# Kernel tuning notes

Measured on AMD Instinct MI355X. Metric: run time of the kernel, lower is better.

The kernel has to match this reference:

```python
import jax, jax.numpy as jnp
import numpy as np

B, A, N = 4, 256, 64
NCB, NF, NSB, DIMS = 128, 128, 50, 3
CUTOFF = 5.0
LOG2 = 0.6931471805599453


def ssp(x):
    # shifted softplus: softplus(x) - ln(2)
    return jax.nn.softplus(x) - LOG2


def mlp2(x, W1, b1, W2, b2):
    # Dense(act=ssp) -> Dense(linear)
    return ssp(x @ W1 + b1) @ W2 + b2


def setup_inputs():
    key = jax.random.key(0)
    ks = jax.random.split(key, 32)

    def w(k, shape):
        return jax.random.normal(k, shape, jnp.float32) / np.sqrt(shape[0]).astype(np.float32)

    return {
        "xi": jax.random.normal(ks[0], (B, A, NCB), jnp.float32),
        "r_ij": jax.random.uniform(ks[1], (B, A, N), jnp.float32) * CUTOFF,
        "cos_ij": jax.random.normal(ks[2], (B, A, N, DIMS), jnp.float32),
        "f_ij": jax.random.normal(ks[3], (B, A, N, NSB), jnp.float32),
        "neighbor_mask": jnp.ones((B, A, N), jnp.float32),
        "filt_W1": w(ks[4], (NSB, NF)), "filt_b1": jnp.zeros((NF,), jnp.float32),
        "filt_W2": w(ks[5], (NF, NF)), "filt_b2": jnp.zeros((NF,), jnp.float32),
        "in2f_W": w(ks[6], (NCB, NF)),
        "f2out_W": w(ks[7], (NF, NF)), "f2out_b": jnp.zeros((NF,), jnp.float32),
        "atom_W1": w(ks[8], (NF, NF)), "atom_b1": jnp.zeros((NF,), jnp.float32),
        "atom_W2": w(ks[9], (NF, NCB)), "atom_b2": jnp.zeros((NCB,), jnp.float32),
        "pair_W1": w(ks[10], (NF, NF)), "pair_b1": jnp.zeros((NF,), jnp.float32),
        "pair_W2": w(ks[11], (NF, NCB)), "pair_b2": jnp.zeros((NCB,), jnp.float32),
        "env_W1": w(ks[12], (NF, NF)), "env_b1": jnp.zeros((NF,), jnp.float32),
        "env_W2": w(ks[13], (NF, NCB)), "env_b2": jnp.zeros((NCB,), jnp.float32),
        "neighbors": jax.random.randint(ks[14], (B, A, N), 0, A),
    }


def reference(xi, r_ij, cos_ij, f_ij, neighbor_mask,
              filt_W1, filt_b1, filt_W2, filt_b2, in2f_W, f2out_W, f2out_b,
              atom_W1, atom_b1, atom_W2, atom_b2,
              pair_W1, pair_b1, pair_W2, pair_b2,
              env_W1, env_b1, env_W2, env_b2, neighbors):
    bidx = jnp.arange(B)[:, None, None]
    # --- FTLayer: filter net on Gaussian-expanded distances, cosine cutoff ---
    Wf = ssp(f_ij @ filt_W1 + filt_b1) @ filt_W2 + filt_b2            # [B,A,N,NF]
    C = 0.5 * (jnp.cos(r_ij * (jnp.pi / CUTOFF)) + 1.0) * (r_ij < CUTOFF)
    Wf = Wf * C[..., None]
    yj = (xi @ in2f_W)[bidx, neighbors]                               # gather -> [B,A,N,NF]
    v = ssp((yj * Wf) @ f2out_W + f2out_b)                            # [B,A,N,NF]
    # --- atom-wise channel (masked neighbor sum) ---
    vi = jnp.sum(v * neighbor_mask[..., None], axis=2)                # [B,A,NF]
    vi = mlp2(vi, atom_W1, atom_b1, atom_W2, atom_b2)                 # [B,A,NCB]
    # --- pair tensor: outer product with cosine basis ---
    vij = mlp2(v, pair_W1, pair_b1, pair_W2, pair_b2)                 # [B,A,N,NCB]
    Vij = vij[..., None] * cos_ij[..., None, :]                       # [B,A,N,NCB,3]
    # --- environment tensor: masked agg then second-order neighbor gather ---
    vik = mlp2(v, env_W1, env_b1, env_W2, env_b2)                     # [B,A,N,NCB]
    Vik = jnp.sum(vik[..., None] * cos_ij[..., None, :]
                  * neighbor_mask[..., None, None], axis=2)           # [B,A,NCB,3]
    Vjl = Vik[bidx, neighbors]                                        # [B,A,N,NCB,3]
    V = Vij + Vik[:, :, None] + Vjl                                   # [B,A,N,NCB,3]
    return vi, V
```

## Files before the change

kernel.cpp:

```cpp
#include <hip/hip_runtime.h>
#include <hip/hip_bf16.h>
#include <math.h>

#define B 4
#define A 256
#define NN 64
#define NCB 128
#define NF 128
#define NSB 50
#define BA (B*A)
#define PAIRS (BA*NN)

typedef __bf16 bf;
typedef __attribute__((ext_vector_type(8))) __bf16 bfrag8;
typedef __attribute__((ext_vector_type(4))) float ffrag4;

__device__ __attribute__((aligned(16))) bf    g_yib[BA*NF];
__device__ __attribute__((aligned(16))) bf    g_vij[(size_t)PAIRS*NCB];
__device__ __attribute__((aligned(16))) float g_vik[BA*NCB*3];
__device__ __attribute__((aligned(16))) bf g_tf1[NF*64];
__device__ __attribute__((aligned(16))) bf g_tf2[NF*NF];
__device__ __attribute__((aligned(16))) bf g_tfo[NF*NF];
__device__ __attribute__((aligned(16))) bf g_tp1[NF*NF];
__device__ __attribute__((aligned(16))) bf g_tp2[NF*NF];
__device__ __attribute__((aligned(16))) bf g_te1[NF*NF];
__device__ __attribute__((aligned(16))) bf g_te2[NF*NF];

__device__ __forceinline__ float ssp(float x){
    float e = __expf(-fabsf(x));
    return fmaxf(x, 0.f) + __logf(1.f + e) - 0.6931471805599453f;
}

__global__ __launch_bounds__(256)
void k_wt(const float* __restrict__ f1, const float* __restrict__ f2,
          const float* __restrict__ fo, const float* __restrict__ p1,
          const float* __restrict__ p2, const float* __restrict__ e1,
          const float* __restrict__ e2){
    int s = blockIdx.x >> 3, part = blockIdx.x & 7;
    const float* src; bf* dst; int kb, realK;
    if (s == 0){ src = f1; dst = g_tf1; kb = 6; realK = NSB; }
    else {
        kb = 7; realK = 128;
        src = (s==1)?f2:(s==2)?fo:(s==3)?p1:(s==4)?p2:(s==5)?e1:e2;
        dst = (s==1)?g_tf2:(s==2)?g_tfo:(s==3)?g_tp1:(s==4)?g_tp2:(s==5)?g_te1:g_te2;
    }
    int total = NF << kb;
    int chunk = total >> 3;
    int end = (part + 1) * chunk;
    for (int e = part*chunk + threadIdx.x; e < end; e += 256){
        int n = e >> kb, k = e & ((1<<kb)-1);
        dst[e] = (k < realK) ? (bf)src[k*NF + n] : (bf)0.f;
    }
}

__global__ __launch_bounds__(NF)
void k_yi(const float* __restrict__ xi, const float* __restrict__ W){
    int row = blockIdx.x, f = threadIdx.x;
    __shared__ float x[NCB];
    x[f] = xi[row*NCB + f];
    __syncthreads();
    float s = 0.f;
    #pragma unroll 16
    for (int c = 0; c < NCB; c++) s += x[c]*W[c*NF + f];
    g_yib[row*NF + f] = (bf)s;
}

__device__ __forceinline__ void stage_w128(bf* __restrict__ sW, const bf* __restrict__ g,
                                           int half, int tid){
    #pragma unroll
    for (int i = 0; i < 4; i++){
        int r  = i*16 + (tid >> 4);
        int cp = (tid & 15)*8;
        *(bfrag8*)&sW[r*136 + cp] = *(const bfrag8*)&g[(half*64 + r)*128 + cp];
    }
}
__device__ __forceinline__ void stage_w64(bf* __restrict__ sW, const bf* __restrict__ g,
                                          int half, int tid){
    #pragma unroll
    for (int i = 0; i < 2; i++){
        int r  = i*32 + (tid >> 3);
        int cp = (tid & 7)*8;
        *(bfrag8*)&sW[r*72 + cp] = *(const bfrag8*)&g[(half*64 + r)*64 + cp];
    }
}
__device__ __forceinline__ void gemm4(const bf* __restrict__ sW, const bfrag8 afr[4],
                                      ffrag4 acc[4], int q, int c16){
    #pragma unroll
    for (int nt = 0; nt < 4; nt++){
        ffrag4 a = {0.f,0.f,0.f,0.f};
        #pragma unroll
        for (int kt = 0; kt < 4; kt++){
            bfrag8 bv = *(const bfrag8*)&sW[(nt*16 + c16)*136 + kt*32 + q*8];
            a = __builtin_amdgcn_mfma_f32_16x16x32_bf16(afr[kt], bv, a, 0, 0, 0);
        }
        acc[nt] = a;
    }
}
__device__ __forceinline__ void gemm2(const bf* __restrict__ sW, const bfrag8 afr[2],
                                      ffrag4 acc[4], int q, int c16){
    #pragma unroll
    for (int nt = 0; nt < 4; nt++){
        ffrag4 a = {0.f,0.f,0.f,0.f};
        #pragma unroll
        for (int kt = 0; kt < 2; kt++){
            bfrag8 bv = *(const bfrag8*)&sW[(nt*16 + c16)*72 + kt*32 + q*8];
            a = __builtin_amdgcn_mfma_f32_16x16x32_bf16(afr[kt], bv, a, 0, 0, 0);
        }
        acc[nt] = a;
    }
}

__global__ __launch_bounds__(256, 3)
void k_main(const float* __restrict__ r_ij, const float* __restrict__ cos_ij,
            const float* __restrict__ f_ij, const float* __restrict__ mask,
            const int* __restrict__ neighbors,
            const float* __restrict__ fb1, const float* __restrict__ fb2,
            const float* __restrict__ f2b,
            const float* __restrict__ aW1, const float* __restrict__ ab1,
            const float* __restrict__ aW2, const float* __restrict__ ab2,
            const float* __restrict__ pb1, const float* __restrict__ pb2,
            const float* __restrict__ eb1, const float* __restrict__ eb2,
            float* __restrict__ out_vi){
    const int tid  = threadIdx.x;
    const int ba   = blockIdx.x;
    const int b    = ba >> 8;
    const int w    = tid >> 6;
    const int lane = tid & 63;
    const int q    = lane >> 4;
    const int c16  = lane & 15;
    const int arow = w*16 + c16;

    __shared__ __attribute__((aligned(16))) char sWb[64*136*2];
    bf* const sW = (bf*)sWb;
    __shared__ __attribute__((aligned(16))) bf sA [64*136];
    __shared__ __attribute__((aligned(16))) bf sA2[64*136];
    __shared__ float sCosM[64*4];
    __shared__ float sCr[64];
    __shared__ int   sJb[64];

    #pragma unroll
    for (int i = 0; i < 16; i++){
        int e = tid + i*256;
        int row = e >> 6, col = e & 63;
        float v = (col < NSB) ? f_ij[(ba*64 + row)*NSB + col] : 0.f;
        sA2[row*136 + col] = (bf)v;
    }
    if (tid < 64){
        int p = ba*64 + tid;
        sCosM[tid*4+0] = cos_ij[p*3+0];
        sCosM[tid*4+1] = cos_ij[p*3+1];
        sCosM[tid*4+2] = cos_ij[p*3+2];
        sCosM[tid*4+3] = mask[p];
        float r = r_ij[p];
        sCr[tid] = (r < 5.f) ? 0.5f*(__cosf(r*0.62831853071795864769f) + 1.f) : 0.f;
        int j = neighbors[p] & (A-1);
        sJb[tid] = (b*A + j)*NF;
    }
    __syncthreads();

    bfrag8 afr4[4]; bfrag8 afr2[2]; ffrag4 acc[4];

    #pragma unroll
    for (int kt = 0; kt < 2; kt++) afr2[kt] = *(const bfrag8*)&sA2[arow*136 + kt*32 + q*8];
    #pragma unroll
    for (int half = 0; half < 2; half++){
        if (half) __syncthreads();
        stage_w64(sW, g_tf1, half, tid);
        __syncthreads();
        gemm2(sW, afr2, acc, q, c16);
        #pragma unroll
        for (int nt = 0; nt < 4; nt++){
            int col = (half*4 + nt)*16 + c16;
            float bias = fb1[col];
            #pragma unroll
            for (int rg = 0; rg < 4; rg++){
                int row = w*16 + q*4 + rg;
                sA[row*136 + col] = (bf)ssp(acc[nt][rg] + bias);
            }
        }
    }
    __syncthreads();

    #pragma unroll
    for (int kt = 0; kt < 4; kt++) afr4[kt] = *(const bfrag8*)&sA[arow*136 + kt*32 + q*8];
    #pragma unroll
    for (int half = 0; half < 2; half++){
        if (half) __syncthreads();
        stage_w128(sW, g_tf2, half, tid);
        __syncthreads();
        gemm4(sW, afr4, acc, q, c16);
        #pragma unroll
        for (int nt = 0; nt < 4; nt++){
            int col = (half*4 + nt)*16 + c16;
            float bias = fb2[col];
            #pragma unroll
            for (int rg = 0; rg < 4; rg++){
                int row = w*16 + q*4 + rg;
                float wf = (acc[nt][rg] + bias) * sCr[row];
                float u  = (float)g_yib[sJb[row] + col] * wf;
                sA[row*136 + col] = (bf)u;
            }
        }
    }
    __syncthreads();

    float vsAll[8];
    #pragma unroll
    for (int t = 0; t < 8; t++) vsAll[t] = 0.f;
    #pragma unroll
    for (int kt = 0; kt < 4; kt++) afr4[kt] = *(const bfrag8*)&sA[arow*136 + kt*32 + q*8];
    #pragma unroll
    for (int half = 0; half < 2; half++){
        if (half) __syncthreads();
        stage_w128(sW, g_tfo, half, tid);
        __syncthreads();
        gemm4(sW, afr4, acc, q, c16);
        #pragma unroll
        for (int nt = 0; nt < 4; nt++){
            int col = (half*4 + nt)*16 + c16;
            float bias = f2b[col];
            #pragma unroll
            for (int rg = 0; rg < 4; rg++){
                int row = w*16 + q*4 + rg;
                float v = ssp(acc[nt][rg] + bias);
                sA[row*136 + col] = (bf)v;
                vsAll[half*4 + nt] += v * sCosM[row*4+3];
            }
        }
    }
    __syncthreads();

    #pragma unroll
    for (int kt = 0; kt < 4; kt++) afr4[kt] = *(const bfrag8*)&sA[arow*136 + kt*32 + q*8];
    #pragma unroll
    for (int half = 0; half < 2; half++){
        if (half) __syncthreads();
        stage_w128(sW, g_tp1, half, tid);
        __syncthreads();
        gemm4(sW, afr4, acc, q, c16);
        #pragma unroll
        for (int nt = 0; nt < 4; nt++){
            int col = (half*4 + nt)*16 + c16;
            float bias = pb1[col];
            #pragma unroll
            for (int rg = 0; rg < 4; rg++){
                int row = w*16 + q*4 + rg;
                sA2[row*136 + col] = (bf)ssp(acc[nt][rg] + bias);
            }
        }
    }
    __syncthreads();

    #pragma unroll
    for (int kt = 0; kt < 4; kt++) afr4[kt] = *(const bfrag8*)&sA2[arow*136 + kt*32 + q*8];
    #pragma unroll
    for (int half = 0; half < 2; half++){
        if (half) __syncthreads();
        stage_w128(sW, g_tp2, half, tid);
        __syncthreads();
        gemm4(sW, afr4, acc, q, c16);
        #pragma unroll
        for (int nt = 0; nt < 4; nt++){
            int col = (half*4 + nt)*16 + c16;
            float bias = pb2[col];
            #pragma unroll
            for (int rg = 0; rg < 4; rg++){
                int row = w*16 + q*4 + rg;
                sA2[row*136 + col] = (bf)(acc[nt][rg] + bias);
            }
        }
    }
    __syncthreads();

    #pragma unroll
    for (int i = 0; i < 4; i++){
        int row = i*16 + (tid >> 4);
        int cp  = (tid & 15)*8;
        *(bfrag8*)&g_vij[((size_t)ba*64 + row)*128 + cp] = *(const bfrag8*)&sA2[row*136 + cp];
    }
    #pragma unroll
    for (int kt = 0; kt < 4; kt++) afr4[kt] = *(const bfrag8*)&sA[arow*136 + kt*32 + q*8];
    #pragma unroll
    for (int half = 0; half < 2; half++){
        if (half) __syncthreads();
        stage_w128(sW, g_te1, half, tid);
        __syncthreads();
        gemm4(sW, afr4, acc, q, c16);
        #pragma unroll
        for (int nt = 0; nt < 4; nt++){
            int col = (half*4 + nt)*16 + c16;
            float bias = eb1[col];
            #pragma unroll
            for (int rg = 0; rg < 4; rg++){
                int row = w*16 + q*4 + rg;
                sA2[row*136 + col] = (bf)ssp(acc[nt][rg] + bias);
            }
        }
    }
    __syncthreads();

    float vkAll[8][3];
    #pragma unroll
    for (int t = 0; t < 8; t++){ vkAll[t][0]=0.f; vkAll[t][1]=0.f; vkAll[t][2]=0.f; }
    #pragma unroll
    for (int kt = 0; kt < 4; kt++) afr4[kt] = *(const bfrag8*)&sA2[arow*136 + kt*32 + q*8];
    #pragma unroll
    for (int half = 0; half < 2; half++){
        if (half) __syncthreads();
        stage_w128(sW, g_te2, half, tid);
        __syncthreads();
        gemm4(sW, afr4, acc, q, c16);
        #pragma unroll
        for (int nt = 0; nt < 4; nt++){
            float bias = eb2[(half*4 + nt)*16 + c16];
            #pragma unroll
            for (int rg = 0; rg < 4; rg++){
                int row = w*16 + q*4 + rg;
                float vik = (acc[nt][rg] + bias) * sCosM[row*4+3];
                vkAll[half*4 + nt][0] += vik * sCosM[row*4+0];
                vkAll[half*4 + nt][1] += vik * sCosM[row*4+1];
                vkAll[half*4 + nt][2] += vik * sCosM[row*4+2];
            }
        }
    }

    __syncthreads();
    float* const sVs   = (float*)sWb;
    float* const sVk   = (float*)(sWb + 2048);
    float* const sVsum = (float*)(sWb + 8192);
    float* const sHa   = (float*)(sWb + 8704);
    #pragma unroll
    for (int t = 0; t < 8; t++){
        float v = vsAll[t];
        v += __shfl_xor(v, 16);
        v += __shfl_xor(v, 32);
        if (q == 0) sVs[w*128 + t*16 + c16] = v;
    }
    #pragma unroll
    for (int t = 0; t < 8; t++){
        #pragma unroll
        for (int d = 0; d < 3; d++){
            float v = vkAll[t][d];
            v += __shfl_xor(v, 16);
            v += __shfl_xor(v, 32);
            if (q == 0) sVk[w*384 + (t*16 + c16)*3 + d] = v;
        }
    }
    __syncthreads();

    for (int e = tid; e < 384; e += 256)
        g_vik[ba*384 + e] = sVk[e] + sVk[384+e] + sVk[768+e] + sVk[1152+e];
    if (tid < 128)
        sVsum[tid] = sVs[tid] + sVs[128+tid] + sVs[256+tid] + sVs[384+tid];
    __syncthreads();
    if (tid < 128){
        float acc2 = ab1[tid];
        #pragma unroll 16
        for (int k = 0; k < 128; k++) acc2 += sVsum[k]*aW1[k*128 + tid];
        sHa[tid] = ssp(acc2);
    }
    __syncthreads();
    if (tid < 128){
        float acc2 = ab2[tid];
        #pragma unroll 16
        for (int k = 0; k < 128; k++) acc2 += sHa[k]*aW2[k*128 + tid];
        out_vi[ba*128 + tid] = acc2;
    }
}

__global__ __launch_bounds__(256)
void k_V(const float* __restrict__ cos_ij, const int* __restrict__ nbrs,
         float* __restrict__ outV){
    const int ba  = blockIdx.x;
    const int b   = ba >> 8;
    const int tid = threadIdx.x;
    const int g   = tid >> 7;
    const int t   = tid & 127;
    __shared__ float sVa[384];
    __shared__ float sC[64*3];
    __shared__ int   sJ[64];
    for (int e = tid; e < 384; e += 256) sVa[e] = g_vik[ba*384 + e];
    if (tid < 64){
        int p = ba*64 + tid;
        sJ[tid] = (b*A + (nbrs[p] & (A-1)))*384;
        sC[tid*3+0] = cos_ij[p*3+0];
        sC[tid*3+1] = cos_ij[p*3+1];
        sC[tid*3+2] = cos_ij[p*3+2];
    }
    __syncthreads();
    const int t3 = t*3;
    const float a0 = sVa[t3+0], a1 = sVa[t3+1], a2 = sVa[t3+2];
    #pragma unroll 2
    for (int i = 0; i < 32; i++){
        int n = i*2 + g;
        size_t p = (size_t)ba*64 + n;
        float vv = (float)g_vij[p*128 + t];
        const float* vjp = g_vik + sJ[n] + t3;
        float c0 = sC[n*3+0], c1 = sC[n*3+1], c2 = sC[n*3+2];
        float* o = outV + p*384 + t3;
        __builtin_nontemporal_store(fmaf(vv, c0, a0 + vjp[0]), o+0);
        __builtin_nontemporal_store(fmaf(vv, c1, a1 + vjp[1]), o+1);
        __builtin_nontemporal_store(fmaf(vv, c2, a2 + vjp[2]), o+2);
    }
}

extern "C" void kernel_launch(void* const* d_in, const int* in_sizes, int n_in,
                              void* d_out, int out_size, void* d_ws, size_t ws_size,
                              hipStream_t stream){
    const float* xi      = (const float*)d_in[0];
    const float* r_ij    = (const float*)d_in[1];
    const float* cos_ij  = (const float*)d_in[2];
    const float* f_ij    = (const float*)d_in[3];
    const float* nmask   = (const float*)d_in[4];
    const float* fW1     = (const float*)d_in[5];
    const float* fb1     = (const float*)d_in[6];
    const float* fW2     = (const float*)d_in[7];
    const float* fb2     = (const float*)d_in[8];
    const float* in2f_W  = (const float*)d_in[9];
    const float* f2W     = (const float*)d_in[10];
    const float* f2b     = (const float*)d_in[11];
    const float* aW1     = (const float*)d_in[12];
    const float* ab1     = (const float*)d_in[13];
    const float* aW2     = (const float*)d_in[14];
    const float* ab2     = (const float*)d_in[15];
    const float* pW1     = (const float*)d_in[16];
    const float* pb1     = (const float*)d_in[17];
    const float* pW2     = (const float*)d_in[18];
    const float* pb2     = (const float*)d_in[19];
    const float* eW1     = (const float*)d_in[20];
    const float* eb1     = (const float*)d_in[21];
    const float* eW2     = (const float*)d_in[22];
    const float* eb2     = (const float*)d_in[23];
    const int*  nbrs     = (const int*)d_in[24];

    float* out_vi = (float*)d_out;
    float* outV   = (float*)d_out + BA*NCB;

    k_wt<<<56, 256, 0, stream>>>(fW1, fW2, f2W, pW1, pW2, eW1, eW2);
    k_yi<<<BA, NF, 0, stream>>>(xi, in2f_W);

    k_main<<<BA, 256, 0, stream>>>(r_ij, cos_ij, f_ij, nmask, nbrs,
                                   fb1, fb2, f2b,
                                   aW1, ab1, aW2, ab2,
                                   pb1, pb2, eb1, eb2,
                                   out_vi);

    k_V<<<BA, 256, 0, stream>>>(cos_ij, nbrs, outV);
}
```

Measured before the change: 258.3 us.

## Prefetch next weight half into registers and vectorize V output kernel

The main kernel now loads the next 64-row weight slice from global memory into registers while the current slice is being multiplied, so the load latency hides behind the MFMA work rather than sitting between barriers. The first filter layer is padded to K=128 so every stage can share one gemm path. The V kernel is also reworked so each lane handles two channels, using packed bf16 loads and float2 loads and stores in place of scalar nontemporal stores. The cost is extra registers, which may hurt occupancy, and some wasted MFMA work on the zero-padded K.

```diff
diff --git a/kernel.cpp b/kernel.cpp
--- a/kernel.cpp
+++ b/kernel.cpp
@@ -18,7 +18,7 @@
 __device__ __attribute__((aligned(16))) bf    g_yib[BA*NF];
 __device__ __attribute__((aligned(16))) bf    g_vij[(size_t)PAIRS*NCB];
 __device__ __attribute__((aligned(16))) float g_vik[BA*NCB*3];
-__device__ __attribute__((aligned(16))) bf g_tf1[NF*64];
+__device__ __attribute__((aligned(16))) bf g_tf1[NF*128];
 __device__ __attribute__((aligned(16))) bf g_tf2[NF*NF];
 __device__ __attribute__((aligned(16))) bf g_tfo[NF*NF];
 __device__ __attribute__((aligned(16))) bf g_tp1[NF*NF];
@@ -37,18 +37,12 @@
           const float* __restrict__ p2, const float* __restrict__ e1,
           const float* __restrict__ e2){
     int s = blockIdx.x >> 3, part = blockIdx.x & 7;
-    const float* src; bf* dst; int kb, realK;
-    if (s == 0){ src = f1; dst = g_tf1; kb = 6; realK = NSB; }
-    else {
-        kb = 7; realK = 128;
-        src = (s==1)?f2:(s==2)?fo:(s==3)?p1:(s==4)?p2:(s==5)?e1:e2;
-        dst = (s==1)?g_tf2:(s==2)?g_tfo:(s==3)?g_tp1:(s==4)?g_tp2:(s==5)?g_te1:g_te2;
-    }
-    int total = NF << kb;
-    int chunk = total >> 3;
-    int end = (part + 1) * chunk;
-    for (int e = part*chunk + threadIdx.x; e < end; e += 256){
-        int n = e >> kb, k = e & ((1<<kb)-1);
+    const float* src = (s==0)?f1:(s==1)?f2:(s==2)?fo:(s==3)?p1:(s==4)?p2:(s==5)?e1:e2;
+    bf* dst = (s==0)?g_tf1:(s==1)?g_tf2:(s==2)?g_tfo:(s==3)?g_tp1:(s==4)?g_tp2:(s==5)?g_te1:g_te2;
+    int realK = (s==0) ? NSB : 128;
+    int base = part*2048;
+    for (int e = base + threadIdx.x; e < base + 2048; e += 256){
+        int n = e >> 7, k = e & 127;
         dst[e] = (k < realK) ? (bf)src[k*NF + n] : (bf)0.f;
     }
 }
@@ -65,22 +59,21 @@
     g_yib[row*NF + f] = (bf)s;
 }
 
-__device__ __forceinline__ void stage_w128(bf* __restrict__ sW, const bf* __restrict__ g,
-                                           int half, int tid){
+__device__ __forceinline__ void wload(bfrag8 r[4], const bf* __restrict__ g,
+                                      int half, int tid){
     #pragma unroll
     for (int i = 0; i < 4; i++){
-        int r  = i*16 + (tid >> 4);
+        int rr = i*16 + (tid >> 4);
         int cp = (tid & 15)*8;
-        *(bfrag8*)&sW[r*136 + cp] = *(const bfrag8*)&g[(half*64 + r)*128 + cp];
-    }
-}
-__device__ __forceinline__ void stage_w64(bf* __restrict__ sW, const bf* __restrict__ g,
-                                          int half, int tid){
-    #pragma unroll
-    for (int i = 0; i < 2; i++){
-        int r  = i*32 + (tid >> 3);
-        int cp = (tid & 7)*8;
-        *(bfrag8*)&sW[r*72 + cp] = *(const bfrag8*)&g[(half*64 + r)*64 + cp];
+        r[i] = *(const bfrag8*)&g[(half*64 + rr)*128 + cp];
+    }
+}
+__device__ __forceinline__ void wstore(bf* __restrict__ sW, const bfrag8 r[4], int tid){
+    #pragma unroll
+    for (int i = 0; i < 4; i++){
+        int rr = i*16 + (tid >> 4);
+        int cp = (tid & 15)*8;
+        *(bfrag8*)&sW[rr*136 + cp] = r[i];
     }
 }
 __device__ __forceinline__ void gemm4(const bf* __restrict__ sW, const bfrag8 afr[4],
@@ -96,19 +89,27 @@
         acc[nt] = a;
     }
 }
-__device__ __forceinline__ void gemm2(const bf* __restrict__ sW, const bfrag8 afr[2],
-                                      ffrag4 acc[4], int q, int c16){
-    #pragma unroll
-    for (int nt = 0; nt < 4; nt++){
-        ffrag4 a = {0.f,0.f,0.f,0.f};
-        #pragma unroll
-        for (int kt = 0; kt < 2; kt++){
-            bfrag8 bv = *(const bfrag8*)&sW[(nt*16 + c16)*72 + kt*32 + q*8];
-            a = __builtin_amdgcn_mfma_f32_16x16x32_bf16(afr[kt], bv, a, 0, 0, 0);
-        }
-        acc[nt] = a;
-    }
-}
+
+#define RDA(SRC) { _Pragma("unroll") for (int kt = 0; kt < 4; kt++) \
+    afr[kt] = *(const bfrag8*)&SRC[arow*136 + kt*32 + q*8]; }
+
+#define EPI_SSP(DST, BIASP, H) \
+    { _Pragma("unroll") for (int nt = 0; nt < 4; nt++){ \
+        int col = ((H)*4 + nt)*16 + c16; \
+        float bias = BIASP[col]; \
+        _Pragma("unroll") for (int rg = 0; rg < 4; rg++){ \
+            int row = w*16 + q*4 + rg; \
+            DST[row*136 + col] = (bf)ssp(acc[nt][rg] + bias); \
+        } } }
+
+#define EPI_LIN(DST, BIASP, H) \
+    { _Pragma("unroll") for (int nt = 0; nt < 4; nt++){ \
+        int col = ((H)*4 + nt)*16 + c16; \
+        float bias = BIASP[col]; \
+        _Pragma("unroll") for (int rg = 0; rg < 4; rg++){ \
+            int row = w*16 + q*4 + rg; \
+            DST[row*136 + col] = (bf)(acc[nt][rg] + bias); \
+        } } }
 
 __global__ __launch_bounds__(256, 3)
 void k_main(const float* __restrict__ r_ij, const float* __restrict__ cos_ij,
@@ -138,10 +139,14 @@
     __shared__ float sCr[64];
     __shared__ int   sJb[64];
 
-    #pragma unroll
-    for (int i = 0; i < 16; i++){
+    bfrag8 wA[4], wB[4], afr[4]; ffrag4 acc[4];
+
+    wload(wA, g_tf1, 0, tid);
+
+    #pragma unroll
+    for (int i = 0; i < 32; i++){
         int e = tid + i*256;
-        int row = e >> 6, col = e & 63;
+        int row = e >> 7, col = e & 127;
         float v = (col < NSB) ? f_ij[(ba*64 + row)*NSB + col] : 0.f;
         sA2[row*136 + col] = (bf)v;
     }
@@ -158,118 +163,101 @@
     }
     __syncthreads();
 
-    bfrag8 afr4[4]; bfrag8 afr2[2]; ffrag4 acc[4];
-
-    #pragma unroll
-    for (int kt = 0; kt < 2; kt++) afr2[kt] = *(const bfrag8*)&sA2[arow*136 + kt*32 + q*8];
-    #pragma unroll
-    for (int half = 0; half < 2; half++){
-        if (half) __syncthreads();
-        stage_w64(sW, g_tf1, half, tid);
-        __syncthreads();
-        gemm2(sW, afr2, acc, q, c16);
-        #pragma unroll
-        for (int nt = 0; nt < 4; nt++){
-            int col = (half*4 + nt)*16 + c16;
-            float bias = fb1[col];
-            #pragma unroll
-            for (int rg = 0; rg < 4; rg++){
-                int row = w*16 + q*4 + rg;
-                sA[row*136 + col] = (bf)ssp(acc[nt][rg] + bias);
-            }
-        }
-    }
-    __syncthreads();
-
-    #pragma unroll
-    for (int kt = 0; kt < 4; kt++) afr4[kt] = *(const bfrag8*)&sA[arow*136 + kt*32 + q*8];
-    #pragma unroll
-    for (int half = 0; half < 2; half++){
-        if (half) __syncthreads();
-        stage_w128(sW, g_tf2, half, tid);
-        __syncthreads();
-        gemm4(sW, afr4, acc, q, c16);
-        #pragma unroll
-        for (int nt = 0; nt < 4; nt++){
-            int col = (half*4 + nt)*16 + c16;
-            float bias = fb2[col];
-            #pragma unroll
-            for (int rg = 0; rg < 4; rg++){
-                int row = w*16 + q*4 + rg;
-                float wf = (acc[nt][rg] + bias) * sCr[row];
-                float u  = (float)g_yib[sJb[row] + col] * wf;
-                sA[row*136 + col] = (bf)u;
-            }
-        }
-    }
+    RDA(sA2);
+
+    wstore(sW, wA, tid); wload(wB, g_tf1, 1, tid); __syncthreads();
+    gemm4(sW, afr, acc, q, c16);
+    EPI_SSP(sA, fb1, 0);
+    __syncthreads();
+    wstore(sW, wB, tid); wload(wA, g_tf2, 0, tid); __syncthreads();
+    gemm4(sW, afr, acc, q, c16);
+    EPI_SSP(sA, fb1, 1);
+    RDA(sA);
+    __syncthreads();
+
+    wstore(sW, wA, tid); wload(wB, g_tf2, 1, tid); __syncthreads();
+    gemm4(sW, afr, acc, q, c16);
+    #pragma unroll
+    for (int nt = 0; nt < 4; nt++){
+        int col = nt*16 + c16;
+        float bias = fb2[col];
+        #pragma unroll
+        for (int rg = 0; rg < 4; rg++){
+            int row = w*16 + q*4 + rg;
+            float wf = (acc[nt][rg] + bias) * sCr[row];
+            sA[row*136 + col] = (bf)((float)g_yib[sJb[row] + col] * wf);
+        }
+    }
+    __syncthreads();
+    wstore(sW, wB, tid); wload(wA, g_tfo, 0, tid); __syncthreads();
+    gemm4(sW, afr, acc, q, c16);
+    #pragma unroll
+    for (int nt = 0; nt < 4; nt++){
+        int col = (4 + nt)*16 + c16;
+        float bias = fb2[col];
+        #pragma unroll
+        for (int rg = 0; rg < 4; rg++){
+            int row = w*16 + q*4 + rg;
+            float wf = (acc[nt][rg] + bias) * sCr[row];
+            sA[row*136 + col] = (bf)((float)g_yib[sJb[row] + col] * wf);
+        }
+    }
+    RDA(sA);
     __syncthreads();
 
     float vsAll[8];
     #pragma unroll
     for (int t = 0; t < 8; t++) vsAll[t] = 0.f;
-    #pragma unroll
-    for (int kt = 0; kt < 4; kt++) afr4[kt] = *(const bfrag8*)&sA[arow*136 + kt*32 + q*8];
-    #pragma unroll
-    for (int half = 0; half < 2; half++){
-        if (half) __syncthreads();
-        stage_w128(sW, g_tfo, half, tid);
-        __syncthreads();
-        gemm4(sW, afr4, acc, q, c16);
-        #pragma unroll
-        for (int nt = 0; nt < 4; nt++){
-            int col = (half*4 + nt)*16 + c16;
-            float bias = f2b[col];
-            #pragma unroll
-            for (int rg = 0; rg < 4; rg++){
-                int row = w*16 + q*4 + rg;
-                float v = ssp(acc[nt][rg] + bias);
-                sA[row*136 + col] = (bf)v;
-                vsAll[half*4 + nt] += v * sCosM[row*4+3];
-            }
-        }
-    }
-    __syncthreads();
-
-    #pragma unroll
-    for (int kt = 0; kt < 4; kt++) afr4[kt] = *(const bfrag8*)&sA[arow*136 + kt*32 + q*8];
-    #pragma unroll
-    for (int half = 0; half < 2; half++){
-        if (half) __syncthreads();
-        stage_w128(sW, g_tp1, half, tid);
-        __syncthreads();
-        gemm4(sW, afr4, acc, q, c16);
-        #pragma unroll
-        for (int nt = 0; nt < 4; nt++){
-            int col = (half*4 + nt)*16 + c16;
-            float bias = pb1[col];
-            #pragma unroll
-            for (int rg = 0; rg < 4; rg++){
-                int row = w*16 + q*4 + rg;
-                sA2[row*136 + col] = (bf)ssp(acc[nt][rg] + bias);
-            }
-        }
-    }
-    __syncthreads();
-
-    #pragma unroll
-    for (int kt = 0; kt < 4; kt++) afr4[kt] = *(const bfrag8*)&sA2[arow*136 + kt*32 + q*8];
-    #pragma unroll
-    for (int half = 0; half < 2; half++){
-        if (half) __syncthreads();
-        stage_w128(sW, g_tp2, half, tid);
-        __syncthreads();
-        gemm4(sW, afr4, acc, q, c16);
-        #pragma unroll
-        for (int nt = 0; nt < 4; nt++){
-            int col = (half*4 + nt)*16 + c16;
-            float bias = pb2[col];
-            #pragma unroll
-            for (int rg = 0; rg < 4; rg++){
-                int row = w*16 + q*4 + rg;
-                sA2[row*136 + col] = (bf)(acc[nt][rg] + bias);
-            }
-        }
-    }
+    wstore(sW, wA, tid); wload(wB, g_tfo, 1, tid); __syncthreads();
+    gemm4(sW, afr, acc, q, c16);
+    #pragma unroll
+    for (int nt = 0; nt < 4; nt++){
+        int col = nt*16 + c16;
+        float bias = f2b[col];
+        #pragma unroll
+        for (int rg = 0; rg < 4; rg++){
+            int row = w*16 + q*4 + rg;
+            float v = ssp(acc[nt][rg] + bias);
+            sA[row*136 + col] = (bf)v;
+            vsAll[nt] += v * sCosM[row*4+3];
+        }
+    }
+    __syncthreads();
+    wstore(sW, wB, tid); wload(wA, g_tp1, 0, tid); __syncthreads();
+    gemm4(sW, afr, acc, q, c16);
+    #pragma unroll
+    for (int nt = 0; nt < 4; nt++){
+        int col = (4 + nt)*16 + c16;
+        float bias = f2b[col];
+        #pragma unroll
+        for (int rg = 0; rg < 4; rg++){
+            int row = w*16 + q*4 + rg;
+            float v = ssp(acc[nt][rg] + bias);
+            sA[row*136 + col] = (bf)v;
+            vsAll[4 + nt] += v * sCosM[row*4+3];
+        }
+    }
+    RDA(sA);
+    __syncthreads();
+
+    wstore(sW, wA, tid); wload(wB, g_tp1, 1, tid); __syncthreads();
+    gemm4(sW, afr, acc, q, c16);
+    EPI_SSP(sA2, pb1, 0);
+    __syncthreads();
+    wstore(sW, wB, tid); wload(wA, g_tp2, 0, tid); __syncthreads();
+    gemm4(sW, afr, acc, q, c16);
+    EPI_SSP(sA2, pb1, 1);
+    RDA(sA2);
+    __syncthreads();
+
+    wstore(sW, wA, tid); wload(wB, g_tp2, 1, tid); __syncthreads();
+    gemm4(sW, afr, acc, q, c16);
+    EPI_LIN(sA2, pb2, 0);
+    __syncthreads();
+    wstore(sW, wB, tid); wload(wA, g_te1, 0, tid); __syncthreads();
+    gemm4(sW, afr, acc, q, c16);
+    EPI_LIN(sA2, pb2, 1);
+    RDA(sA);
     __syncthreads();
 
     #pragma unroll
@@ -278,49 +266,46 @@
         int cp  = (tid & 15)*8;
         *(bfrag8*)&g_vij[((size_t)ba*64 + row)*128 + cp] = *(const bfrag8*)&sA2[row*136 + cp];
     }
-    #pragma unroll
-    for (int kt = 0; kt < 4; kt++) afr4[kt] = *(const bfrag8*)&sA[arow*136 + kt*32 + q*8];
-    #pragma unroll
-    for (int half = 0; half < 2; half++){
-        if (half) __syncthreads();
-        stage_w128(sW, g_te1, half, tid);
-        __syncthreads();
-        gemm4(sW, afr4, acc, q, c16);
-        #pragma unroll
-        for (int nt = 0; nt < 4; nt++){
-            int col = (half*4 + nt)*16 + c16;
-            float bias = eb1[col];
-            #pragma unroll
-            for (int rg = 0; rg < 4; rg++){
-                int row = w*16 + q*4 + rg;
-                sA2[row*136 + col] = (bf)ssp(acc[nt][rg] + bias);
-            }
-        }
-    }
+    wstore(sW, wA, tid); wload(wB, g_te1, 1, tid); __syncthreads();
+    gemm4(sW, afr, acc, q, c16);
+    EPI_SSP(sA2, eb1, 0);
+    __syncthreads();
+    wstore(sW, wB, tid); wload(wA, g_te2, 0, tid); __syncthreads();
+    gemm4(sW, afr, acc, q, c16);
+    EPI_SSP(sA2, eb1, 1);
+    RDA(sA2);
     __syncthreads();
 
     float vkAll[8][3];
     #pragma unroll
     for (int t = 0; t < 8; t++){ vkAll[t][0]=0.f; vkAll[t][1]=0.f; vkAll[t][2]=0.f; }
-    #pragma unroll
-    for (int kt = 0; kt < 4; kt++) afr4[kt] = *(const bfrag8*)&sA2[arow*136 + kt*32 + q*8];
-    #pragma unroll
-    for (int half = 0; half < 2; half++){
-        if (half) __syncthreads();
-        stage_w128(sW, g_te2, half, tid);
-        __syncthreads();
-        gemm4(sW, afr4, acc, q, c16);
-        #pragma unroll
-        for (int nt = 0; nt < 4; nt++){
-            float bias = eb2[(half*4 + nt)*16 + c16];
-            #pragma unroll
-            for (int rg = 0; rg < 4; rg++){
-                int row = w*16 + q*4 + rg;
-                float vik = (acc[nt][rg] + bias) * sCosM[row*4+3];
-                vkAll[half*4 + nt][0] += vik * sCosM[row*4+0];
-                vkAll[half*4 + nt][1] += vik * sCosM[row*4+1];
-                vkAll[half*4 + nt][2] += vik * sCosM[row*4+2];
-            }
+    wstore(sW, wA, tid); wload(wB, g_te2, 1, tid); __syncthreads();
+    gemm4(sW, afr, acc, q, c16);
+    #pragma unroll
+    for (int nt = 0; nt < 4; nt++){
+        float bias = eb2[nt*16 + c16];
+        #pragma unroll
+        for (int rg = 0; rg < 4; rg++){
+            int row = w*16 + q*4 + rg;
+            float vik = (acc[nt][rg] + bias) * sCosM[row*4+3];
+            vkAll[nt][0] += vik * sCosM[row*4+0];
+            vkAll[nt][1] += vik * sCosM[row*4+1];
+            vkAll[nt][2] += vik * sCosM[row*4+2];
+        }
+    }
+    __syncthreads();
+    wstore(sW, wB, tid); __syncthreads();
+    gemm4(sW, afr, acc, q, c16);
+    #pragma unroll
+    for (int nt = 0; nt < 4; nt++){
+        float bias = eb2[(4 + nt)*16 + c16];
+        #pragma unroll
+        for (int rg = 0; rg < 4; rg++){
+            int row = w*16 + q*4 + rg;
+            float vik = (acc[nt][rg] + bias) * sCosM[row*4+3];
+            vkAll[4 + nt][0] += vik * sCosM[row*4+0];
+            vkAll[4 + nt][1] += vik * sCosM[row*4+1];
+            vkAll[4 + nt][2] += vik * sCosM[row*4+2];
         }
     }
 
@@ -371,36 +356,45 @@
 __global__ __launch_bounds__(256)
 void k_V(const float* __restrict__ cos_ij, const int* __restrict__ nbrs,
          float* __restrict__ outV){
-    const int ba  = blockIdx.x;
-    const int b   = ba >> 8;
-    const int tid = threadIdx.x;
-    const int g   = tid >> 7;
-    const int t   = tid & 127;
+    const int ba   = blockIdx.x;
+    const int b    = ba >> 8;
+    const int tid  = threadIdx.x;
+    const int w    = tid >> 6;
+    const int lane = tid & 63;
     __shared__ float sVa[384];
-    __shared__ float sC[64*3];
+    __shared__ float sC[64*4];
     __shared__ int   sJ[64];
     for (int e = tid; e < 384; e += 256) sVa[e] = g_vik[ba*384 + e];
     if (tid < 64){
         int p = ba*64 + tid;
         sJ[tid] = (b*A + (nbrs[p] & (A-1)))*384;
-        sC[tid*3+0] = cos_ij[p*3+0];
-        sC[tid*3+1] = cos_ij[p*3+1];
-        sC[tid*3+2] = cos_ij[p*3+2];
-    }
-    __syncthreads();
-    const int t3 = t*3;
-    const float a0 = sVa[t3+0], a1 = sVa[t3+1], a2 = sVa[t3+2];
-    #pragma unroll 2
-    for (int i = 0; i < 32; i++){
-        int n = i*2 + g;
+        sC[tid*4+0] = cos_ij[p*3+0];
+        sC[tid*4+1] = cos_ij[p*3+1];
+        sC[tid*4+2] = cos_ij[p*3+2];
+    }
+    __syncthreads();
+    const int c0 = lane*2;
+    const float a00=sVa[c0*3+0], a01=sVa[c0*3+1], a02=sVa[c0*3+2];
+    const float a10=sVa[c0*3+3], a11=sVa[c0*3+4], a12=sVa[c0*3+5];
+    #pragma unroll 4
+    for (int i = 0; i < 16; i++){
+        int n = w*16 + i;
         size_t p = (size_t)ba*64 + n;
-        float vv = (float)g_vij[p*128 + t];
-        const float* vjp = g_vik + sJ[n] + t3;
-        float c0 = sC[n*3+0], c1 = sC[n*3+1], c2 = sC[n*3+2];
-        float* o = outV + p*384 + t3;
-        __builtin_nontemporal_store(fmaf(vv, c0, a0 + vjp[0]), o+0);
-        __builtin_nontemporal_store(fmaf(vv, c1, a1 + vjp[1]), o+1);
-        __builtin_nontemporal_store(fmaf(vv, c2, a2 + vjp[2]), o+2);
+        unsigned int u = *(const unsigned int*)&g_vij[p*128 + c0];
+        float v0 = __uint_as_float(u << 16);
+        float v1 = __uint_as_float(u & 0xffff0000u);
+        float cc0 = sC[n*4+0], cc1 = sC[n*4+1], cc2 = sC[n*4+2];
+        const float* vj = g_vik + sJ[n] + c0*3;
+        float2 j01 = *(const float2*)(vj);
+        float2 j23 = *(const float2*)(vj + 2);
+        float2 j45 = *(const float2*)(vj + 4);
+        float* o = outV + p*384 + c0*3;
+        float2 o01 = { fmaf(v0, cc0, a00 + j01.x), fmaf(v0, cc1, a01 + j01.y) };
+        float2 o23 = { fmaf(v0, cc2, a02 + j23.x), fmaf(v1, cc0, a10 + j23.y) };
+        float2 o45 = { fmaf(v1, cc1, a11 + j45.x), fmaf(v1, cc2, a12 + j45.y) };
+        *(float2*)(o)     = o01;
+        *(float2*)(o + 2) = o23;
+        *(float2*)(o + 4) = o45;
     }
 }
 
```

New measurement: 285.4 us. 10.5% more time.

## Read MFMA weights from global directly, drop LDS staging and block barriers

Applied to the files above, without the earlier changes.

The main kernel no longer stages each weight half into shared memory between block barriers. Each wave now reads B fragments for all 8 column tiles straight from global/L2, and each wave handles only its own 16 rows, so the chain runs without __syncthreads. Dropping the weight buffer frees LDS, so launch bounds go from 3 to 4 blocks per CU. The V kernel is reworked to stage g_vij in LDS and write the output with fully coalesced flat indexing, in place of strided 3-element stores. The cost is more global/L2 traffic for weights on every fragment load, with possible latency stalls.

```diff
diff --git a/kernel.cpp b/kernel.cpp
--- a/kernel.cpp
+++ b/kernel.cpp
@@ -65,52 +65,25 @@
     g_yib[row*NF + f] = (bf)s;
 }
 
-__device__ __forceinline__ void stage_w128(bf* __restrict__ sW, const bf* __restrict__ g,
-                                           int half, int tid){
-    #pragma unroll
-    for (int i = 0; i < 4; i++){
-        int r  = i*16 + (tid >> 4);
-        int cp = (tid & 15)*8;
-        *(bfrag8*)&sW[r*136 + cp] = *(const bfrag8*)&g[(half*64 + r)*128 + cp];
-    }
-}
-__device__ __forceinline__ void stage_w64(bf* __restrict__ sW, const bf* __restrict__ g,
-                                          int half, int tid){
-    #pragma unroll
-    for (int i = 0; i < 2; i++){
-        int r  = i*32 + (tid >> 3);
-        int cp = (tid & 7)*8;
-        *(bfrag8*)&sW[r*72 + cp] = *(const bfrag8*)&g[(half*64 + r)*64 + cp];
-    }
-}
-__device__ __forceinline__ void gemm4(const bf* __restrict__ sW, const bfrag8 afr[4],
-                                      ffrag4 acc[4], int q, int c16){
-    #pragma unroll
-    for (int nt = 0; nt < 4; nt++){
+template<int NKT, class EPI>
+__device__ __forceinline__ void stageG(const bf* __restrict__ gW,
+                                       const bfrag8* afr, int c16, int q, EPI epi){
+    #pragma unroll
+    for (int nt = 0; nt < 8; nt++){
         ffrag4 a = {0.f,0.f,0.f,0.f};
         #pragma unroll
-        for (int kt = 0; kt < 4; kt++){
-            bfrag8 bv = *(const bfrag8*)&sW[(nt*16 + c16)*136 + kt*32 + q*8];
+        for (int kt = 0; kt < NKT; kt++){
+            bfrag8 bv = *(const bfrag8*)&gW[(nt*16 + c16)*(NKT*32) + kt*32 + q*8];
             a = __builtin_amdgcn_mfma_f32_16x16x32_bf16(afr[kt], bv, a, 0, 0, 0);
         }
-        acc[nt] = a;
-    }
-}
-__device__ __forceinline__ void gemm2(const bf* __restrict__ sW, const bfrag8 afr[2],
-                                      ffrag4 acc[4], int q, int c16){
-    #pragma unroll
-    for (int nt = 0; nt < 4; nt++){
-        ffrag4 a = {0.f,0.f,0.f,0.f};
-        #pragma unroll
-        for (int kt = 0; kt < 2; kt++){
-            bfrag8 bv = *(const bfrag8*)&sW[(nt*16 + c16)*72 + kt*32 + q*8];
-            a = __builtin_amdgcn_mfma_f32_16x16x32_bf16(afr[kt], bv, a, 0, 0, 0);
-        }
-        acc[nt] = a;
-    }
-}
-
-__global__ __launch_bounds__(256, 3)
+        epi(nt, a);
+    }
+}
+
+#define RDA4(SRC) { _Pragma("unroll") for (int kt = 0; kt < 4; kt++) \
+    afr[kt] = *(const bfrag8*)&SRC[arow*136 + kt*32 + q*8]; }
+
+__global__ __launch_bounds__(256, 4)
 void k_main(const float* __restrict__ r_ij, const float* __restrict__ cos_ij,
             const float* __restrict__ f_ij, const float* __restrict__ mask,
             const int* __restrict__ neighbors,
@@ -130,8 +103,6 @@
     const int c16  = lane & 15;
     const int arow = w*16 + c16;
 
-    __shared__ __attribute__((aligned(16))) char sWb[64*136*2];
-    bf* const sW = (bf*)sWb;
     __shared__ __attribute__((aligned(16))) bf sA [64*136];
     __shared__ __attribute__((aligned(16))) bf sA2[64*136];
     __shared__ float sCosM[64*4];
@@ -140,195 +111,125 @@
 
     #pragma unroll
     for (int i = 0; i < 16; i++){
-        int e = tid + i*256;
-        int row = e >> 6, col = e & 63;
-        float v = (col < NSB) ? f_ij[(ba*64 + row)*NSB + col] : 0.f;
-        sA2[row*136 + col] = (bf)v;
-    }
-    if (tid < 64){
-        int p = ba*64 + tid;
-        sCosM[tid*4+0] = cos_ij[p*3+0];
-        sCosM[tid*4+1] = cos_ij[p*3+1];
-        sCosM[tid*4+2] = cos_ij[p*3+2];
-        sCosM[tid*4+3] = mask[p];
+        int row = w*16 + i;
+        float v = (lane < NSB) ? f_ij[(ba*64 + row)*NSB + lane] : 0.f;
+        sA2[row*136 + lane] = (bf)v;
+    }
+    if (lane < 16){
+        int row = w*16 + lane;
+        int p = ba*64 + row;
+        sCosM[row*4+0] = cos_ij[p*3+0];
+        sCosM[row*4+1] = cos_ij[p*3+1];
+        sCosM[row*4+2] = cos_ij[p*3+2];
+        sCosM[row*4+3] = mask[p];
         float r = r_ij[p];
-        sCr[tid] = (r < 5.f) ? 0.5f*(__cosf(r*0.62831853071795864769f) + 1.f) : 0.f;
+        sCr[row] = (r < 5.f) ? 0.5f*(__cosf(r*0.62831853071795864769f) + 1.f) : 0.f;
         int j = neighbors[p] & (A-1);
-        sJb[tid] = (b*A + j)*NF;
-    }
-    __syncthreads();
-
-    bfrag8 afr4[4]; bfrag8 afr2[2]; ffrag4 acc[4];
-
-    #pragma unroll
-    for (int kt = 0; kt < 2; kt++) afr2[kt] = *(const bfrag8*)&sA2[arow*136 + kt*32 + q*8];
-    #pragma unroll
-    for (int half = 0; half < 2; half++){
-        if (half) __syncthreads();
-        stage_w64(sW, g_tf1, half, tid);
-        __syncthreads();
-        gemm2(sW, afr2, acc, q, c16);
-        #pragma unroll
-        for (int nt = 0; nt < 4; nt++){
-            int col = (half*4 + nt)*16 + c16;
-            float bias = fb1[col];
-            #pragma unroll
-            for (int rg = 0; rg < 4; rg++){
-                int row = w*16 + q*4 + rg;
-                sA[row*136 + col] = (bf)ssp(acc[nt][rg] + bias);
-            }
-        }
-    }
-    __syncthreads();
-
-    #pragma unroll
-    for (int kt = 0; kt < 4; kt++) afr4[kt] = *(const bfrag8*)&sA[arow*136 + kt*32 + q*8];
-    #pragma unroll
-    for (int half = 0; half < 2; half++){
-        if (half) __syncthreads();
-        stage_w128(sW, g_tf2, half, tid);
-        __syncthreads();
-        gemm4(sW, afr4, acc, q, c16);
-        #pragma unroll
-        for (int nt = 0; nt < 4; nt++){
-            int col = (half*4 + nt)*16 + c16;
-            float bias = fb2[col];
-            #pragma unroll
-            for (int rg = 0; rg < 4; rg++){
-                int row = w*16 + q*4 + rg;
-                float wf = (acc[nt][rg] + bias) * sCr[row];
-                float u  = (float)g_yib[sJb[row] + col] * wf;
-                sA[row*136 + col] = (bf)u;
-            }
-        }
-    }
-    __syncthreads();
+        sJb[row] = (b*A + j)*NF;
+    }
+
+    bfrag8 afr[4];
+
+    #pragma unroll
+    for (int kt = 0; kt < 2; kt++) afr[kt] = *(const bfrag8*)&sA2[arow*136 + kt*32 + q*8];
+    stageG<2>(g_tf1, afr, c16, q, [&](int nt, ffrag4 a){
+        int col = nt*16 + c16;
+        float bias = fb1[col];
+        #pragma unroll
+        for (int rg = 0; rg < 4; rg++){
+            int row = w*16 + q*4 + rg;
+            sA[row*136 + col] = (bf)ssp(a[rg] + bias);
+        }
+    });
+
+    RDA4(sA);
+    stageG<4>(g_tf2, afr, c16, q, [&](int nt, ffrag4 a){
+        int col = nt*16 + c16;
+        float bias = fb2[col];
+        #pragma unroll
+        for (int rg = 0; rg < 4; rg++){
+            int row = w*16 + q*4 + rg;
+            float wf = (a[rg] + bias) * sCr[row];
+            sA[row*136 + col] = (bf)((float)g_yib[sJb[row] + col] * wf);
+        }
+    });
 
     float vsAll[8];
     #pragma unroll
     for (int t = 0; t < 8; t++) vsAll[t] = 0.f;
-    #pragma unroll
-    for (int kt = 0; kt < 4; kt++) afr4[kt] = *(const bfrag8*)&sA[arow*136 + kt*32 + q*8];
-    #pragma unroll
-    for (int half = 0; half < 2; half++){
-        if (half) __syncthreads();
-        stage_w128(sW, g_tfo, half, tid);
-        __syncthreads();
-        gemm4(sW, afr4, acc, q, c16);
-        #pragma unroll
-        for (int nt = 0; nt < 4; nt++){
-            int col = (half*4 + nt)*16 + c16;
-            float bias = f2b[col];
-            #pragma unroll
-            for (int rg = 0; rg < 4; rg++){
-                int row = w*16 + q*4 + rg;
-                float v = ssp(acc[nt][rg] + bias);
-                sA[row*136 + col] = (bf)v;
-                vsAll[half*4 + nt] += v * sCosM[row*4+3];
-            }
-        }
-    }
-    __syncthreads();
-
-    #pragma unroll
-    for (int kt = 0; kt < 4; kt++) afr4[kt] = *(const bfrag8*)&sA[arow*136 + kt*32 + q*8];
-    #pragma unroll
-    for (int half = 0; half < 2; half++){
-        if (half) __syncthreads();
-        stage_w128(sW, g_tp1, half, tid);
-        __syncthreads();
-        gemm4(sW, afr4, acc, q, c16);
-        #pragma unroll
-        for (int nt = 0; nt < 4; nt++){
-            int col = (half*4 + nt)*16 + c16;
-            float bias = pb1[col];
-            #pragma unroll
-            for (int rg = 0; rg < 4; rg++){
-                int row = w*16 + q*4 + rg;
-                sA2[row*136 + col] = (bf)ssp(acc[nt][rg] + bias);
-            }
-        }
-    }
-    __syncthreads();
-
-    #pragma unroll
-    for (int kt = 0; kt < 4; kt++) afr4[kt] = *(const bfrag8*)&sA2[arow*136 + kt*32 + q*8];
-    #pragma unroll
-    for (int half = 0; half < 2; half++){
-        if (half) __syncthreads();
-        stage_w128(sW, g_tp2, half, tid);
-        __syncthreads();
-        gemm4(sW, afr4, acc, q, c16);
-        #pragma unroll
-        for (int nt = 0; nt < 4; nt++){
-            int col = (half*4 + nt)*16 + c16;
-            float bias = pb2[col];
-            #pragma unroll
-            for (int rg = 0; rg < 4; rg++){
-                int row = w*16 + q*4 + rg;
-                sA2[row*136 + col] = (bf)(acc[nt][rg] + bias);
-            }
-        }
-    }
-    __syncthreads();
+    RDA4(sA);
+    stageG<4>(g_tfo, afr, c16, q, [&](int nt, ffrag4 a){
+        int col = nt*16 + c16;
+        float bias = f2b[col];
+        #pragma unroll
+        for (int rg = 0; rg < 4; rg++){
+            int row = w*16 + q*4 + rg;
+            float v = ssp(a[rg] + bias);
+            sA[row*136 + col] = (bf)v;
+            vsAll[nt] += v * sCosM[row*4+3];
+        }
+    });
+
+    RDA4(sA);
+    stageG<4>(g_tp1, afr, c16, q, [&](int nt, ffrag4 a){
+        int col = nt*16 + c16;
+        float bias = pb1[col];
+        #pragma unroll
+        for (int rg = 0; rg < 4; rg++){
+            int row = w*16 + q*4 + rg;
+            sA2[row*136 + col] = (bf)ssp(a[rg] + bias);
+        }
+    });
+
+    RDA4(sA2);
+    stageG<4>(g_tp2, afr, c16, q, [&](int nt, ffrag4 a){
+        int col = nt*16 + c16;
+        float bias = pb2[col];
+        #pragma unroll
+        for (int rg = 0; rg < 4; rg++){
+            int row = w*16 + q*4 + rg;
+            sA2[row*136 + col] = (bf)(a[rg] + bias);
+        }
+    });
 
     #pragma unroll
     for (int i = 0; i < 4; i++){
-        int row = i*16 + (tid >> 4);
-        int cp  = (tid & 15)*8;
+        int row = w*16 + i*4 + (lane >> 4);
+        int cp  = c16*8;
         *(bfrag8*)&g_vij[((size_t)ba*64 + row)*128 + cp] = *(const bfrag8*)&sA2[row*136 + cp];
     }
-    #pragma unroll
-    for (int kt = 0; kt < 4; kt++) afr4[kt] = *(const bfrag8*)&sA[arow*136 + kt*32 + q*8];
-    #pragma unroll
-    for (int half = 0; half < 2; half++){
-        if (half) __syncthreads();
-        stage_w128(sW, g_te1, half, tid);
-        __syncthreads();
-        gemm4(sW, afr4, acc, q, c16);
-        #pragma unroll
-        for (int nt = 0; nt < 4; nt++){
-            int col = (half*4 + nt)*16 + c16;
-            float bias = eb1[col];
-            #pragma unroll
-            for (int rg = 0; rg < 4; rg++){
-                int row = w*16 + q*4 + rg;
-                sA2[row*136 + col] = (bf)ssp(acc[nt][rg] + bias);
-            }
-        }
-    }
-    __syncthreads();
+    RDA4(sA);
+    stageG<4>(g_te1, afr, c16, q, [&](int nt, ffrag4 a){
+        int col = nt*16 + c16;
+        float bias = eb1[col];
+        #pragma unroll
+        for (int rg = 0; rg < 4; rg++){
+            int row = w*16 + q*4 + rg;
+            sA2[row*136 + col] = (bf)ssp(a[rg] + bias);
+        }
+    });
 
     float vkAll[8][3];
     #pragma unroll
     for (int t = 0; t < 8; t++){ vkAll[t][0]=0.f; vkAll[t][1]=0.f; vkAll[t][2]=0.f; }
-    #pragma unroll
-    for (int kt = 0; kt < 4; kt++) afr4[kt] = *(const bfrag8*)&sA2[arow*136 + kt*32 + q*8];
-    #pragma unroll
-    for (int half = 0; half < 2; half++){
-        if (half) __syncthreads();
-        stage_w128(sW, g_te2, half, tid);
-        __syncthreads();
-        gemm4(sW, afr4, acc, q, c16);
-        #pragma unroll
-        for (int nt = 0; nt < 4; nt++){
-            float bias = eb2[(half*4 + nt)*16 + c16];
-            #pragma unroll
-            for (int rg = 0; rg < 4; rg++){
-                int row = w*16 + q*4 + rg;
-                float vik = (acc[nt][rg] + bias) * sCosM[row*4+3];
-                vkAll[half*4 + nt][0] += vik * sCosM[row*4+0];
-                vkAll[half*4 + nt][1] += vik * sCosM[row*4+1];
-                vkAll[half*4 + nt][2] += vik * sCosM[row*4+2];
-            }
-        }
-    }
-
-    __syncthreads();
-    float* const sVs   = (float*)sWb;
-    float* const sVk   = (float*)(sWb + 2048);
-    float* const sVsum = (float*)(sWb + 8192);
-    float* const sHa   = (float*)(sWb + 8704);
+    RDA4(sA2);
+    stageG<4>(g_te2, afr, c16, q, [&](int nt, ffrag4 a){
+        float bias = eb2[nt*16 + c16];
+        #pragma unroll
+        for (int rg = 0; rg < 4; rg++){
+            int row = w*16 + q*4 + rg;
+            float vik = (a[rg] + bias) * sCosM[row*4+3];
+            vkAll[nt][0] += vik * sCosM[row*4+0];
+            vkAll[nt][1] += vik * sCosM[row*4+1];
+            vkAll[nt][2] += vik * sCosM[row*4+2];
+        }
+    });
+
+    __syncthreads();
+    float* const sVs   = (float*)sA;
+    float* const sVk   = (float*)((char*)sA + 2048);
+    float* const sVsum = (float*)((char*)sA + 8192);
+    float* const sHa   = (float*)((char*)sA + 8704);
     #pragma unroll
     for (int t = 0; t < 8; t++){
         float v = vsAll[t];
@@ -374,33 +275,35 @@
     const int ba  = blockIdx.x;
     const int b   = ba >> 8;
     const int tid = threadIdx.x;
-    const int g   = tid >> 7;
-    const int t   = tid & 127;
+    __shared__ __attribute__((aligned(16))) bf sVij[64*128];
     __shared__ float sVa[384];
-    __shared__ float sC[64*3];
+    __shared__ float sC[64*4];
     __shared__ int   sJ[64];
+    #pragma unroll
+    for (int i = 0; i < 4; i++){
+        int e8 = tid + i*256;
+        *(bfrag8*)&sVij[e8*8] = *(const bfrag8*)&g_vij[(size_t)ba*8192 + e8*8];
+    }
     for (int e = tid; e < 384; e += 256) sVa[e] = g_vik[ba*384 + e];
     if (tid < 64){
         int p = ba*64 + tid;
         sJ[tid] = (b*A + (nbrs[p] & (A-1)))*384;
-        sC[tid*3+0] = cos_ij[p*3+0];
-        sC[tid*3+1] = cos_ij[p*3+1];
-        sC[tid*3+2] = cos_ij[p*3+2];
-    }
-    __syncthreads();
-    const int t3 = t*3;
-    const float a0 = sVa[t3+0], a1 = sVa[t3+1], a2 = sVa[t3+2];
-    #pragma unroll 2
-    for (int i = 0; i < 32; i++){
-        int n = i*2 + g;
-        size_t p = (size_t)ba*64 + n;
-        float vv = (float)g_vij[p*128 + t];
-        const float* vjp = g_vik + sJ[n] + t3;
-        float c0 = sC[n*3+0], c1 = sC[n*3+1], c2 = sC[n*3+2];
-        float* o = outV + p*384 + t3;
-        __builtin_nontemporal_store(fmaf(vv, c0, a0 + vjp[0]), o+0);
-        __builtin_nontemporal_store(fmaf(vv, c1, a1 + vjp[1]), o+1);
-        __builtin_nontemporal_store(fmaf(vv, c2, a2 + vjp[2]), o+2);
+        sC[tid*4+0] = cos_ij[p*3+0];
+        sC[tid*4+1] = cos_ij[p*3+1];
+        sC[tid*4+2] = cos_ij[p*3+2];
+    }
+    __syncthreads();
+    float* const oBase = outV + (size_t)ba*24576;
+    #pragma unroll 4
+    for (int it = 0; it < 96; it++){
+        int E  = it*256 + tid;
+        int pl = E / 384;
+        int e  = E - pl*384;
+        int c  = e / 3;
+        int d  = e - c*3;
+        float vv  = (float)sVij[pl*128 + c];
+        float val = fmaf(vv, sC[pl*4+d], sVa[e] + g_vik[sJ[pl] + e]);
+        __builtin_nontemporal_store(val, oBase + E);
     }
 }
 
```

New measurement: 296.3 us. 14.7% more time.
